# Kernel tuning notes

Hardware: AMD Instinct MI355X
Metric: run time of the kernel (lower is better)

## Reference

```python
import jax, jax.numpy as jnp
import numpy as np

N = 50000          # nodes
E = 1600000        # edges (avg degree 32)
G = 16             # graphs in batch
H = 128            # hidden_dim
HOP = 3
IN_DIM = 1


def setup_inputs() -> dict:
    key = jax.random.key(0)
    ks = jax.random.split(key, 12)
    s = 1.0 / np.sqrt(H)
    return {
        "x": jax.random.normal(ks[0], (N, IN_DIM), jnp.float32),
        "edge_index": jax.random.randint(ks[1], (2, E), 0, N, jnp.int64),
        "edge_attr": jax.random.uniform(ks[2], (E, 1), jnp.float32),
        "batch": jnp.sort(jax.random.randint(ks[3], (N,), 0, G, jnp.int64)),
        "W1": jax.random.normal(ks[4], (HOP, H, IN_DIM), jnp.float32) * s,
        "W2": jax.random.normal(ks[5], (HOP, H, H), jnp.float32) * s,
        "W3": jax.random.normal(ks[6], (HOP, H, H), jnp.float32) * s,
        "W4": jax.random.normal(ks[7], (HOP, H, 1), jnp.float32) * s,
        "W5": jax.random.normal(ks[8], (1, 2 * H), jnp.float32) * s,
        "b5": jnp.zeros((1,), jnp.float32),
        "W6": jax.random.normal(ks[9], (H, H), jnp.float32) * s,
        "W7": jax.random.normal(ks[10], (H, H), jnp.float32) * s,
    }


def reference(x, edge_index, edge_attr, batch, W1, W2, W3, W4, W5, b5, W6, W7):
    row, col = edge_index[0], edge_index[1]
    node_emb = jnp.zeros((N, H), x.dtype)
    for l in range(HOP):
        nfe = x @ W1[l].T                                        # [N,H]
        # gather neighbor embeddings along col, scatter-add to row
        ne_aggr = jax.ops.segment_sum(node_emb[col], row, num_segments=N)
        efe = jax.nn.relu(edge_attr @ W4[l].T)                   # [E,H]
        ee_aggr = jax.ops.segment_sum(efe, row, num_segments=N)  # [N,H]
        node_emb = jax.nn.relu(nfe + ne_aggr @ W2[l].T + ee_aggr @ W3[l].T)
    pooled = jax.ops.segment_sum(node_emb, batch, num_segments=G)  # [G,H]
    sum_emb = pooled @ W6.T                                        # [G,H]
    cat = jax.nn.relu(jnp.concatenate([sum_emb[batch], node_emb @ W7.T], axis=-1))
    return cat @ W5.T + b5                                         # [N,1]
```

## Files before the change

### kernel.cpp

```cpp
#include <hip/hip_runtime.h>
#include <hip/hip_bf16.h>

#define N_NODES 50000
#define N_EDGES 1600000
#define NGRAPH  16
#define HID     128

#define RPB   128
#define NB    ((N_NODES + RPB - 1) / RPB)
#define NBLK  256
#define EPB   ((N_EDGES + NBLK - 1) / NBLK)
#define P4CAP 6144

typedef unsigned int uint32;
typedef unsigned short ushort;
typedef unsigned char uchar;
typedef __attribute__((ext_vector_type(8))) short bf16x8;
typedef __attribute__((ext_vector_type(4))) float f32x4;
typedef __attribute__((ext_vector_type(2))) float f32x2;

__device__ __forceinline__ uint32 bf16r(float f) {
    uint32 b = __float_as_uint(f);
    return (b + 0x7fffu + ((b >> 16) & 1u)) >> 16;
}
__device__ __forceinline__ uint32 pack_bf16(float lo, float hi) {
    return bf16r(lo) | (bf16r(hi) << 16);
}

__global__ __launch_bounds__(1024) void k_p1i(const int* __restrict__ row,
                                              int* __restrict__ blkhist,
                                              float* __restrict__ zp, int nz,
                                              const float* __restrict__ W2,
                                              const float* __restrict__ W7,
                                              const float* __restrict__ W3,
                                              const float* __restrict__ W4,
                                              ushort* __restrict__ wpack,
                                              float* __restrict__ v3) {
    __shared__ int hist[NB];
    int tid = threadIdx.x, blk = blockIdx.x;
    int gid = blk * 1024 + tid;
    if (gid < nz) zp[gid] = 0.f;
    if (gid < 4 * 16384) {
        int m = gid >> 14, f = gid & 16383;
        int j = f & 7, lane = (f >> 3) & 63, kk = (f >> 9) & 3, t = (f >> 11) & 7;
        int hp = t * 16 + (lane & 15);
        int k  = kk * 32 + ((lane >> 4) & 3) * 8 + j;
        const float* src = (m < 3) ? (W2 + m * HID * HID) : W7;
        wpack[gid] = (ushort)bf16r(src[hp * HID + k]);
    }
    if (gid < 3 * HID) {
        int l = gid / HID, hp = gid % HID;
        float acc = 0.f;
        for (int h = 0; h < HID; h++)
            acc += W3[l * HID * HID + hp * HID + h] * fmaxf(W4[l * HID + h], 0.f);
        v3[gid] = acc;
    }
    for (int i = tid; i < NB; i += 1024) hist[i] = 0;
    __syncthreads();
    int s = blk * EPB, e = s + EPB; if (e > N_EDGES) e = N_EDGES;
    for (int i = s + tid; i < e; i += 1024)
        atomicAdd(&hist[row[i] >> 7], 1);
    __syncthreads();
    for (int i = tid; i < NB; i += 1024)
        blkhist[i * NBLK + blk] = hist[i];
}

__global__ __launch_bounds__(NBLK) void k_p2a(int* __restrict__ blkhist,
                                              int* __restrict__ btot) {
    __shared__ int sums[NBLK];
    int t = threadIdx.x, b = blockIdx.x;
    int v = blkhist[b * NBLK + t];
    sums[t] = v;
    __syncthreads();
    for (int d = 1; d < NBLK; d <<= 1) {
        int u = (t >= d) ? sums[t - d] : 0;
        __syncthreads();
        sums[t] += u;
        __syncthreads();
    }
    blkhist[b * NBLK + t] = sums[t] - v;
    if (t == NBLK - 1) btot[b] = sums[t];
}

__global__ __launch_bounds__(1024) void k_p3_part(const int* __restrict__ row,
                                                  const int* __restrict__ col,
                                                  const float* __restrict__ ea,
                                                  const int* __restrict__ blkhist,
                                                  const int* __restrict__ btot,
                                                  int2* __restrict__ pea) {
    __shared__ int sc[512];
    __shared__ int cur[NB];
    int tid = threadIdx.x, blk = blockIdx.x;
    if (tid < 512) sc[tid] = (tid < NB) ? btot[tid] : 0;
    __syncthreads();
    for (int d = 1; d < 512; d <<= 1) {
        int v = 0;
        if (tid < 512 && tid >= d) v = sc[tid - d];
        __syncthreads();
        if (tid < 512) sc[tid] += v;
        __syncthreads();
    }
    for (int i = tid; i < NB; i += 1024)
        cur[i] = (sc[i] - btot[i]) + blkhist[i * NBLK + blk];
    __syncthreads();
    int s = blk * EPB, e = s + EPB; if (e > N_EDGES) e = N_EDGES;
    for (int i = s + tid; i < e; i += 1024) {
        int r = row[i], c = col[i];
        float a = ea[i];
        int slot = atomicAdd(&cur[r >> 7], 1);
        pea[slot] = make_int2(((r & (RPB - 1)) << 16) | c, __float_as_int(a));
    }
}

__global__ __launch_bounds__(512) void k_p4(const int2* __restrict__ pea,
                                            const int* __restrict__ btot,
                                            const float* __restrict__ x,
                                            int* __restrict__ offs,
                                            float* __restrict__ ea_sum,
                                            int* __restrict__ csr,
                                            uchar* __restrict__ emb0,
                                            const float* __restrict__ w1l0,
                                            const float* __restrict__ v3l0) {
    __shared__ int2  cache[P4CAP];
    __shared__ int   red[512];
    __shared__ int   cnt[RPB];
    __shared__ float eas[RPB];
    __shared__ int   scan_s[RPB];
    __shared__ int   curp[RPB];
    int t = threadIdx.x, b = blockIdx.x;
    red[t] = (t < b) ? btot[t] : 0;
    __syncthreads();
    for (int d = 256; d > 0; d >>= 1) {
        if (t < d) red[t] += red[t + d];
        __syncthreads();
    }
    int s = red[0];
    int e = s + btot[b];
    int len = e - s;
    int clen = len < P4CAP ? len : P4CAP;
    for (int i = t; i < clen; i += 512) cache[i] = pea[s + i];
    if (t < RPB) { cnt[t] = 0; eas[t] = 0.f; }
    __syncthreads();
    for (int i = t; i < len; i += 512) {
        int2 p = (i < P4CAP) ? cache[i] : pea[s + i];
        int lr = ((uint32)p.x) >> 16;
        atomicAdd(&cnt[lr], 1);
        atomicAdd(&eas[lr], __int_as_float(p.y));
    }
    __syncthreads();
    if (t < RPB) scan_s[t] = cnt[t];
    __syncthreads();
    for (int d = 1; d < RPB; d <<= 1) {
        int v = 0;
        if (t < RPB && t >= d) v = scan_s[t - d];
        __syncthreads();
        if (t < RPB) scan_s[t] += v;
        __syncthreads();
    }
    int nbase = b * RPB;
    if (t < RPB) {
        int excl = scan_s[t] - cnt[t];
        int n = nbase + t;
        if (n < N_NODES) {
            offs[n] = s + excl;
            ea_sum[n] = eas[t];
        }
        curp[t] = s + excl;
    }
    if (b == NB - 1 && t == 0) offs[N_NODES] = e;
    __syncthreads();
    for (int i = t; i < len; i += 512) {
        int2 p = (i < P4CAP) ? cache[i] : pea[s + i];
        int slot = atomicAdd(&curp[((uint32)p.x) >> 16], 1);
        csr[slot] = p.x & 0xFFFF;
    }
    for (int i = t; i < RPB * 32; i += 512) {
        int lr = i >> 5, c4 = (i & 31) * 4;
        int n = nbase + lr;
        if (n < N_NODES) {
            float xv = x[n];
            float ev = eas[lr];
            float v0 = fmaxf(xv * w1l0[c4 + 0] + ev * v3l0[c4 + 0], 0.f) * 0.015625f;
            float v1 = fmaxf(xv * w1l0[c4 + 1] + ev * v3l0[c4 + 1], 0.f) * 0.015625f;
            float v2 = fmaxf(xv * w1l0[c4 + 2] + ev * v3l0[c4 + 2], 0.f) * 0.015625f;
            float v3v = fmaxf(xv * w1l0[c4 + 3] + ev * v3l0[c4 + 3], 0.f) * 0.015625f;
            int u = __builtin_amdgcn_cvt_pk_fp8_f32(v0, v1, 0, false);
            u = __builtin_amdgcn_cvt_pk_fp8_f32(v2, v3v, u, true);
            *(uint32*)(emb0 + (size_t)n * 128 + c4) = (uint32)u;
        }
    }
}

__global__ __launch_bounds__(256) void k_gather(const uchar* __restrict__ emb,
                                                const int* __restrict__ offs,
                                                const int* __restrict__ csr,
                                                uint32* __restrict__ agg) {
    int node = (blockIdx.x * 256 + threadIdx.x) >> 6;
    int lane = threadIdx.x & 63;
    if (node >= N_NODES) return;
    int hl = lane & 31;
    int half = lane >> 5;
    int boff = hl << 2;
    int s = offs[node], e = offs[node + 1];
    f32x2 a0 = {0.f, 0.f}, a1 = a0, a2 = a0, a3 = a0;
#pragma unroll 1
    for (int base = s; base < e; base += 64) {
        int idx = base + lane;
        int cv = (idx < e) ? csr[idx] : 0;
        int cnt = e - base; if (cnt > 64) cnt = 64;
        int j = 0;
#pragma unroll 1
        for (; j + 16 <= cnt; j += 16) {
            uint32 w[8];
#pragma unroll
            for (int q = 0; q < 8; q++) {
                int c0 = __builtin_amdgcn_readlane(cv, j + 2 * q);
                int c1 = __builtin_amdgcn_readlane(cv, j + 2 * q + 1);
                int c  = half ? c1 : c0;
                w[q] = *(const uint32*)(emb + (((uint32)c) << 7) + boff);
            }
#pragma unroll
            for (int q = 0; q < 8; q++) {
                f32x2 lo = __builtin_amdgcn_cvt_pk_f32_fp8((int)w[q], false);
                f32x2 hi = __builtin_amdgcn_cvt_pk_f32_fp8((int)w[q], true);
                if (q & 1) { a2 += lo; a3 += hi; } else { a0 += lo; a1 += hi; }
            }
        }
#pragma unroll 1
        for (; j + 2 <= cnt; j += 2) {
            int c0 = __builtin_amdgcn_readlane(cv, j);
            int c1 = __builtin_amdgcn_readlane(cv, j + 1);
            int c  = half ? c1 : c0;
            uint32 w = *(const uint32*)(emb + (((uint32)c) << 7) + boff);
            a0 += __builtin_amdgcn_cvt_pk_f32_fp8((int)w, false);
            a1 += __builtin_amdgcn_cvt_pk_f32_fp8((int)w, true);
        }
        if (j < cnt) {
            int c0 = __builtin_amdgcn_readlane(cv, j);
            uint32 w = half ? 0u : *(const uint32*)(emb + (((uint32)c0) << 7) + boff);
            a0 += __builtin_amdgcn_cvt_pk_f32_fp8((int)w, false);
            a1 += __builtin_amdgcn_cvt_pk_f32_fp8((int)w, true);
        }
    }
    a0 += a2; a1 += a3;
    a0.x += __shfl_xor(a0.x, 32); a0.y += __shfl_xor(a0.y, 32);
    a1.x += __shfl_xor(a1.x, 32); a1.y += __shfl_xor(a1.y, 32);
    if (half == 0) {
        uint2 wv2;
        wv2.x = pack_bf16(a0.x * 64.f, a0.y * 64.f);
        wv2.y = pack_bf16(a1.x * 64.f, a1.y * 64.f);
        *(uint2*)(agg + (size_t)node * 64 + hl * 2) = wv2;
    }
}

#define LROW 136

template <bool LAST>
__global__ __launch_bounds__(256) void k_gemm(const uint32* __restrict__ agg,
                                              const ushort* __restrict__ w2p,
                                              const float* __restrict__ w1l,
                                              const float* __restrict__ v3l,
                                              const float* __restrict__ x,
                                              const float* __restrict__ ea_sum,
                                              uchar* __restrict__ emb8Out,
                                              const ushort* __restrict__ w7p,
                                              const float* __restrict__ W5,
                                              float* __restrict__ outp,
                                              const int* __restrict__ batch,
                                              float* __restrict__ pooled) {
    __shared__ ushort tile[64 * LROW];
    __shared__ float redp[4][128];
    int tid = threadIdx.x;
    int tbase = blockIdx.x * 64;
    int wv = tid >> 6, lane = tid & 63;
    int n0 = lane & 15, quad = lane >> 4;
    int arow = wv * 16 + n0;
    bf16x8 a0 = {0,0,0,0,0,0,0,0}, a1 = a0, a2 = a0, a3 = a0;
    if (tbase + arow < N_NODES) {
        const bf16x8* ap = (const bf16x8*)(agg + (size_t)(tbase + arow) * 64);
        a0 = ap[0 + quad]; a1 = ap[4 + quad]; a2 = ap[8 + quad]; a3 = ap[12 + quad];
    }
    const bf16x8* wb = (const bf16x8*)w2p;
    f32x4 acc[8];
#pragma unroll
    for (int t = 0; t < 8; t++) {
        f32x4 c = {0.f, 0.f, 0.f, 0.f};
        c = __builtin_amdgcn_mfma_f32_16x16x32_bf16(a0, wb[(t * 4 + 0) * 64 + lane], c, 0, 0, 0);
        c = __builtin_amdgcn_mfma_f32_16x16x32_bf16(a1, wb[(t * 4 + 1) * 64 + lane], c, 0, 0, 0);
        c = __builtin_amdgcn_mfma_f32_16x16x32_bf16(a2, wb[(t * 4 + 2) * 64 + lane], c, 0, 0, 0);
        c = __builtin_amdgcn_mfma_f32_16x16x32_bf16(a3, wb[(t * 4 + 3) * 64 + lane], c, 0, 0, 0);
        acc[t] = c;
    }
    float xs[4], es[4];
#pragma unroll
    for (int r = 0; r < 4; r++) {
        int n = tbase + wv * 16 + quad * 4 + r;
        xs[r] = (n < N_NODES) ? x[n] : 0.f;
        es[r] = (n < N_NODES) ? ea_sum[n] : 0.f;
    }
    if (!LAST) {
        uchar* stile = (uchar*)tile;
#pragma unroll
        for (int t = 0; t < 8; t++) {
            int hp = t * 16 + n0;
            float w1v = w1l[hp], v3v = v3l[hp];
#pragma unroll
            for (int r = 0; r < 4; r++) {
                float v = fmaxf(acc[t][r] + xs[r] * w1v + es[r] * v3v, 0.f) * 0.015625f;
                int enc = __builtin_amdgcn_cvt_pk_fp8_f32(v, v, 0, false);
                stile[(wv * 16 + quad * 4 + r) * 136 + hp] = (uchar)(enc & 0xff);
            }
        }
        __syncthreads();
        int vn = N_NODES - tbase; if (vn > 64) vn = 64;
        for (int i = tid; i < 64 * 32; i += 256) {
            int r = i >> 5, c4 = (i & 31) * 4;
            if (r < vn) {
                uint32 u = *(const uint32*)&stile[r * 136 + c4];
                *(uint32*)(emb8Out + (size_t)(tbase + r) * 128 + c4) = u;
            }
        }
    } else {
        int nlast = tbase + 63; if (nlast > N_NODES - 1) nlast = N_NODES - 1;
        int g0 = batch[tbase];
        bool uni = (batch[nlast] == g0);
        int gr[4];
        if (!uni) {
#pragma unroll
            for (int r = 0; r < 4; r++) {
                int n = tbase + wv * 16 + quad * 4 + r;
                gr[r] = (n < N_NODES) ? batch[n] : 0;
            }
        }
        float st[8];
#pragma unroll
        for (int t = 0; t < 8; t++) {
            int hp = t * 16 + n0;
            float w1v = w1l[hp], v3v = v3l[hp];
            float stt = 0.f;
#pragma unroll
            for (int r = 0; r < 4; r++) {
                float v = fmaxf(acc[t][r] + xs[r] * w1v + es[r] * v3v, 0.f);
                tile[(wv * 16 + quad * 4 + r) * LROW + hp] = (ushort)bf16r(v);
                if (uni) {
                    stt += v;
                } else {
                    int n = tbase + wv * 16 + quad * 4 + r;
                    if (n < N_NODES) atomicAdd(&pooled[gr[r] * HID + hp], v);
                }
            }
            st[t] = stt;
        }
        if (uni) {
#pragma unroll
            for (int t = 0; t < 8; t++) {
                float v = st[t];
                v += __shfl_xor(v, 16);
                v += __shfl_xor(v, 32);
                if (lane < 16) redp[wv][t * 16 + lane] = v;
            }
        }
        __syncthreads();
        if (uni && tid < 128) {
            float sp = (redp[0][tid] + redp[1][tid]) + (redp[2][tid] + redp[3][tid]);
            atomicAdd(&pooled[g0 * HID + tid], sp);
        }
        bf16x8 b0 = *(const bf16x8*)&tile[arow * LROW + 0 * 32 + quad * 8];
        bf16x8 b1 = *(const bf16x8*)&tile[arow * LROW + 1 * 32 + quad * 8];
        bf16x8 b2 = *(const bf16x8*)&tile[arow * LROW + 2 * 32 + quad * 8];
        bf16x8 b3 = *(const bf16x8*)&tile[arow * LROW + 3 * 32 + quad * 8];
        const bf16x8* w7 = (const bf16x8*)w7p;
        float p[4] = {0.f, 0.f, 0.f, 0.f};
#pragma unroll
        for (int t = 0; t < 8; t++) {
            f32x4 c = {0.f, 0.f, 0.f, 0.f};
            c = __builtin_amdgcn_mfma_f32_16x16x32_bf16(b0, w7[(t * 4 + 0) * 64 + lane], c, 0, 0, 0);
            c = __builtin_amdgcn_mfma_f32_16x16x32_bf16(b1, w7[(t * 4 + 1) * 64 + lane], c, 0, 0, 0);
            c = __builtin_amdgcn_mfma_f32_16x16x32_bf16(b2, w7[(t * 4 + 2) * 64 + lane], c, 0, 0, 0);
            c = __builtin_amdgcn_mfma_f32_16x16x32_bf16(b3, w7[(t * 4 + 3) * 64 + lane], c, 0, 0, 0);
            float w5v = W5[128 + t * 16 + n0];
#pragma unroll
            for (int r = 0; r < 4; r++) p[r] += fmaxf(c[r], 0.f) * w5v;
        }
#pragma unroll
        for (int r = 0; r < 4; r++) {
            float v = p[r];
            v += __shfl_xor(v, 1);
            v += __shfl_xor(v, 2);
            v += __shfl_xor(v, 4);
            v += __shfl_xor(v, 8);
            int n = tbase + wv * 16 + quad * 4 + r;
            if (n0 == 0 && n < N_NODES) outp[n] = v;
        }
    }
}

__global__ __launch_bounds__(256) void k_tail(float* __restrict__ out,
                                              const int* __restrict__ batch,
                                              const float* __restrict__ pooled,
                                              const float* __restrict__ W6,
                                              const float* __restrict__ W5,
                                              const float* __restrict__ b5) {
    __shared__ float red[256];
    __shared__ int gsh[2];
    int t = threadIdx.x;
    int nbase = blockIdx.x * 256;
    int n = nbase + t;
    if (t == 0) gsh[0] = batch[nbase < N_NODES ? nbase : N_NODES - 1];
    if (t == 1) gsh[1] = batch[(nbase + 255) < N_NODES ? (nbase + 255) : N_NODES - 1];
    __syncthreads();
    int g_lo = gsh[0], g_hi = gsh[1];
    int hp = t & 127;
    int g = (t >> 7) ? g_hi : g_lo;
    const float* pg = pooled + g * HID;
    const float* wr = W6 + hp * HID;
    float acc = 0.f;
    for (int h = 0; h < HID; h++) acc += pg[h] * wr[h];
    red[t] = fmaxf(acc, 0.f) * W5[hp];
    __syncthreads();
    for (int d = 64; d > 0; d >>= 1) {
        if (hp < d) red[t] += red[t + d];
        __syncthreads();
    }
    float s_lo = red[0], s_hi = red[128];
    if (n < N_NODES) {
        int gn = batch[n];
        float s;
        if (gn == g_lo) s = s_lo;
        else if (gn == g_hi) s = s_hi;
        else {
            s = 0.f;
            const float* pg2 = pooled + gn * HID;
            for (int hp2 = 0; hp2 < HID; hp2++) {
                float a2 = 0.f;
                for (int h = 0; h < HID; h++) a2 += pg2[h] * W6[hp2 * HID + h];
                s += fmaxf(a2, 0.f) * W5[hp2];
            }
        }
        out[n] += s + b5[0];
    }
}

extern "C" void kernel_launch(void* const* d_in, const int* in_sizes, int n_in,
                              void* d_out, int out_size, void* d_ws, size_t ws_size,
                              hipStream_t stream) {
    (void)in_sizes; (void)n_in; (void)out_size; (void)ws_size;
    const float* x    = (const float*)d_in[0];
    const int*   ei   = (const int*)d_in[1];
    const float* ea   = (const float*)d_in[2];
    const int*   bat  = (const int*)d_in[3];
    const float* W1   = (const float*)d_in[4];
    const float* W2   = (const float*)d_in[5];
    const float* W3   = (const float*)d_in[6];
    const float* W4   = (const float*)d_in[7];
    const float* W5   = (const float*)d_in[8];
    const float* b5   = (const float*)d_in[9];
    const float* W6   = (const float*)d_in[10];
    const float* W7   = (const float*)d_in[11];
    float* out = (float*)d_out;

    const int* row = ei;
    const int* col = ei + N_EDGES;

    float* wsf = (float*)d_ws;
    int*   wsi = (int*)d_ws;
    size_t o = 0;
    float* pooled = wsf + o; o += NGRAPH * HID;
    size_t ztot = o;
    int*   offs   = wsi + o; o += N_NODES + 1;
    float* ea_sum = wsf + o; o += N_NODES;
    int*   btot   = wsi + o; o += NB;
    float* v3     = wsf + o; o += 3 * HID;
    int*   blkh   = wsi + o; o += NB * NBLK;
    o = (o + 3) & ~(size_t)3;
    ushort* wpack = (ushort*)(wsi + o); o += 4 * 16384 / 2;
    int*    csr   = wsi + o; o += N_EDGES;
    o = (o + 1) & ~(size_t)1;
    int2*   pea   = (int2*)(wsi + o); o += 2 * (size_t)N_EDGES;
    uint32* aggB  = (uint32*)(wsi + o); o += (size_t)N_NODES * 64;
    uchar*  emb8  = (uchar*)(wsi + o);  o += (size_t)N_NODES * 32;
    uchar*  emb0  = (uchar*)(wsi + o);  o += (size_t)N_NODES * 32;

    const ushort* w2p1 = wpack + 1 * 16384;
    const ushort* w2p2 = wpack + 2 * 16384;
    const ushort* w7p  = wpack + 3 * 16384;

    k_p1i<<<NBLK, 1024, 0, stream>>>(row, blkh, (float*)d_ws, (int)ztot,
                                     W2, W7, W3, W4, (ushort*)wpack, v3);
    k_p2a<<<NB, NBLK, 0, stream>>>(blkh, btot);
    k_p3_part<<<NBLK, 1024, 0, stream>>>(row, col, ea, blkh, btot, pea);
    k_p4<<<NB, 512, 0, stream>>>(pea, btot, x, offs, ea_sum, csr, emb0, W1, v3);
    k_gather<<<(N_NODES * 64 + 255) / 256, 256, 0, stream>>>(emb0, offs, csr, aggB);
    k_gemm<false><<<(N_NODES + 63) / 64, 256, 0, stream>>>(
        aggB, w2p1, W1 + 1 * HID, v3 + 1 * HID, x, ea_sum, emb8, nullptr, nullptr, nullptr,
        nullptr, nullptr);
    k_gather<<<(N_NODES * 64 + 255) / 256, 256, 0, stream>>>(emb8, offs, csr, aggB);
    k_gemm<true><<<(N_NODES + 63) / 64, 256, 0, stream>>>(
        aggB, w2p2, W1 + 2 * HID, v3 + 2 * HID, x, ea_sum, nullptr, w7p, W5, out, bat, pooled);
    k_tail<<<(N_NODES + 255) / 256, 256, 0, stream>>>(out, bat, pooled, W6, W5, b5);
}
```

Measured before the change: 266.7 us.

## Split fp8 embeddings into two 64-byte halves and gather each half separately

Node embeddings move from one 128-byte row per node to two separate 3.2 MB arrays holding the low and high 64 features. The gather kernel makes two passes, one per half, with 16 lanes per neighbor, so four neighbors are fetched per wave instruction. Each pass touches a smaller array that fits better in L2/MALL, aiming for a higher cache hit rate on the random neighbor reads. The cost is reading the CSR twice, an extra shuffle-reduction level, and a branchier tail loop.

```diff
diff --git a/kernel.cpp b/kernel.cpp
--- a/kernel.cpp
+++ b/kernel.cpp
@@ -118,7 +118,8 @@
                                             int* __restrict__ offs,
                                             float* __restrict__ ea_sum,
                                             int* __restrict__ csr,
-                                            uchar* __restrict__ emb0,
+                                            uchar* __restrict__ emb0Lo,
+                                            uchar* __restrict__ emb0Hi,
                                             const float* __restrict__ w1l0,
                                             const float* __restrict__ v3l0) {
     __shared__ int2  cache[P4CAP];
@@ -186,70 +187,83 @@
             float v3v = fmaxf(xv * w1l0[c4 + 3] + ev * v3l0[c4 + 3], 0.f) * 0.015625f;
             int u = __builtin_amdgcn_cvt_pk_fp8_f32(v0, v1, 0, false);
             u = __builtin_amdgcn_cvt_pk_fp8_f32(v2, v3v, u, true);
-            *(uint32*)(emb0 + (size_t)n * 128 + c4) = (uint32)u;
-        }
-    }
-}
-
-__global__ __launch_bounds__(256) void k_gather(const uchar* __restrict__ emb,
+            uchar* dst = (c4 < 64) ? emb0Lo : emb0Hi;
+            *(uint32*)(dst + (size_t)n * 64 + (c4 & 63)) = (uint32)u;
+        }
+    }
+}
+
+__global__ __launch_bounds__(256) void k_gather(const uchar* __restrict__ embLo,
+                                                const uchar* __restrict__ embHi,
                                                 const int* __restrict__ offs,
                                                 const int* __restrict__ csr,
                                                 uint32* __restrict__ agg) {
     int node = (blockIdx.x * 256 + threadIdx.x) >> 6;
     int lane = threadIdx.x & 63;
     if (node >= N_NODES) return;
-    int hl = lane & 31;
-    int half = lane >> 5;
-    int boff = hl << 2;
+    int q  = lane >> 4;
+    int ql = lane & 15;
+    int boff = ql << 2;
+    bool q0 = (q & 1) != 0, q1 = (q & 2) != 0;
     int s = offs[node], e = offs[node + 1];
-    f32x2 a0 = {0.f, 0.f}, a1 = a0, a2 = a0, a3 = a0;
 #pragma unroll 1
-    for (int base = s; base < e; base += 64) {
-        int idx = base + lane;
-        int cv = (idx < e) ? csr[idx] : 0;
-        int cnt = e - base; if (cnt > 64) cnt = 64;
-        int j = 0;
+    for (int p = 0; p < 2; p++) {
+        const uchar* emb = p ? embHi : embLo;
+        f32x2 a0 = {0.f, 0.f}, a1 = a0, a2 = a0, a3 = a0;
 #pragma unroll 1
-        for (; j + 16 <= cnt; j += 16) {
-            uint32 w[8];
-#pragma unroll
-            for (int q = 0; q < 8; q++) {
-                int c0 = __builtin_amdgcn_readlane(cv, j + 2 * q);
-                int c1 = __builtin_amdgcn_readlane(cv, j + 2 * q + 1);
-                int c  = half ? c1 : c0;
-                w[q] = *(const uint32*)(emb + (((uint32)c) << 7) + boff);
-            }
-#pragma unroll
-            for (int q = 0; q < 8; q++) {
-                f32x2 lo = __builtin_amdgcn_cvt_pk_f32_fp8((int)w[q], false);
-                f32x2 hi = __builtin_amdgcn_cvt_pk_f32_fp8((int)w[q], true);
-                if (q & 1) { a2 += lo; a3 += hi; } else { a0 += lo; a1 += hi; }
-            }
-        }
+        for (int base = s; base < e; base += 64) {
+            int idx = base + lane;
+            int cv = (idx < e) ? csr[idx] : 0;
+            int cnt = e - base; if (cnt > 64) cnt = 64;
+            int j = 0;
 #pragma unroll 1
-        for (; j + 2 <= cnt; j += 2) {
-            int c0 = __builtin_amdgcn_readlane(cv, j);
-            int c1 = __builtin_amdgcn_readlane(cv, j + 1);
-            int c  = half ? c1 : c0;
-            uint32 w = *(const uint32*)(emb + (((uint32)c) << 7) + boff);
-            a0 += __builtin_amdgcn_cvt_pk_f32_fp8((int)w, false);
-            a1 += __builtin_amdgcn_cvt_pk_f32_fp8((int)w, true);
-        }
-        if (j < cnt) {
-            int c0 = __builtin_amdgcn_readlane(cv, j);
-            uint32 w = half ? 0u : *(const uint32*)(emb + (((uint32)c0) << 7) + boff);
-            a0 += __builtin_amdgcn_cvt_pk_f32_fp8((int)w, false);
-            a1 += __builtin_amdgcn_cvt_pk_f32_fp8((int)w, true);
-        }
-    }
-    a0 += a2; a1 += a3;
-    a0.x += __shfl_xor(a0.x, 32); a0.y += __shfl_xor(a0.y, 32);
-    a1.x += __shfl_xor(a1.x, 32); a1.y += __shfl_xor(a1.y, 32);
-    if (half == 0) {
-        uint2 wv2;
-        wv2.x = pack_bf16(a0.x * 64.f, a0.y * 64.f);
-        wv2.y = pack_bf16(a1.x * 64.f, a1.y * 64.f);
-        *(uint2*)(agg + (size_t)node * 64 + hl * 2) = wv2;
+            for (; j + 16 <= cnt; j += 16) {
+                uint32 w[4];
+#pragma unroll
+                for (int u = 0; u < 4; u++) {
+                    int c0 = __builtin_amdgcn_readlane(cv, j + 4 * u + 0);
+                    int c1 = __builtin_amdgcn_readlane(cv, j + 4 * u + 1);
+                    int c2 = __builtin_amdgcn_readlane(cv, j + 4 * u + 2);
+                    int c3 = __builtin_amdgcn_readlane(cv, j + 4 * u + 3);
+                    int clo = q0 ? c1 : c0;
+                    int chi = q0 ? c3 : c2;
+                    int c   = q1 ? chi : clo;
+                    w[u] = *(const uint32*)(emb + (((uint32)c) << 6) + boff);
+                }
+#pragma unroll
+                for (int u = 0; u < 4; u++) {
+                    f32x2 lo = __builtin_amdgcn_cvt_pk_f32_fp8((int)w[u], false);
+                    f32x2 hi = __builtin_amdgcn_cvt_pk_f32_fp8((int)w[u], true);
+                    if (u & 1) { a2 += lo; a3 += hi; } else { a0 += lo; a1 += hi; }
+                }
+            }
+#pragma unroll 1
+            for (; j < cnt; j += 4) {
+                int jm = cnt - 1;
+                int c0 = __builtin_amdgcn_readlane(cv, j);
+                int c1 = __builtin_amdgcn_readlane(cv, (j + 1 < cnt) ? j + 1 : jm);
+                int c2 = __builtin_amdgcn_readlane(cv, (j + 2 < cnt) ? j + 2 : jm);
+                int c3 = __builtin_amdgcn_readlane(cv, (j + 3 < cnt) ? j + 3 : jm);
+                int clo = q0 ? c1 : c0;
+                int chi = q0 ? c3 : c2;
+                int c   = q1 ? chi : clo;
+                uint32 w = *(const uint32*)(emb + (((uint32)c) << 6) + boff);
+                if (j + q >= cnt) w = 0u;
+                a0 += __builtin_amdgcn_cvt_pk_f32_fp8((int)w, false);
+                a1 += __builtin_amdgcn_cvt_pk_f32_fp8((int)w, true);
+            }
+        }
+        a0 += a2; a1 += a3;
+        a0.x += __shfl_xor(a0.x, 16); a0.y += __shfl_xor(a0.y, 16);
+        a1.x += __shfl_xor(a1.x, 16); a1.y += __shfl_xor(a1.y, 16);
+        a0.x += __shfl_xor(a0.x, 32); a0.y += __shfl_xor(a0.y, 32);
+        a1.x += __shfl_xor(a1.x, 32); a1.y += __shfl_xor(a1.y, 32);
+        if (lane < 16) {
+            uint2 wv2;
+            wv2.x = pack_bf16(a0.x * 64.f, a0.y * 64.f);
+            wv2.y = pack_bf16(a1.x * 64.f, a1.y * 64.f);
+            *(uint2*)(agg + (size_t)node * 64 + p * 32 + ql * 2) = wv2;
+        }
     }
 }
 
@@ -262,7 +276,8 @@
                                               const float* __restrict__ v3l,
                                               const float* __restrict__ x,
                                               const float* __restrict__ ea_sum,
-                                              uchar* __restrict__ emb8Out,
+                                              uchar* __restrict__ emb8Lo,
+                                              uchar* __restrict__ emb8Hi,
                                               const ushort* __restrict__ w7p,
                                               const float* __restrict__ W5,
                                               float* __restrict__ outp,
@@ -317,7 +332,8 @@
             int r = i >> 5, c4 = (i & 31) * 4;
             if (r < vn) {
                 uint32 u = *(const uint32*)&stile[r * 136 + c4];
-                *(uint32*)(emb8Out + (size_t)(tbase + r) * 128 + c4) = u;
+                uchar* dst = (c4 < 64) ? emb8Lo : emb8Hi;
+                *(uint32*)(dst + (size_t)(tbase + r) * 64 + (c4 & 63)) = u;
             }
         }
     } else {
@@ -478,8 +494,10 @@
     o = (o + 1) & ~(size_t)1;
     int2*   pea   = (int2*)(wsi + o); o += 2 * (size_t)N_EDGES;
     uint32* aggB  = (uint32*)(wsi + o); o += (size_t)N_NODES * 64;
-    uchar*  emb8  = (uchar*)(wsi + o);  o += (size_t)N_NODES * 32;
-    uchar*  emb0  = (uchar*)(wsi + o);  o += (size_t)N_NODES * 32;
+    uchar*  emb8Lo = (uchar*)(wsi + o); o += (size_t)N_NODES * 16;
+    uchar*  emb8Hi = (uchar*)(wsi + o); o += (size_t)N_NODES * 16;
+    uchar*  emb0Lo = (uchar*)(wsi + o); o += (size_t)N_NODES * 16;
+    uchar*  emb0Hi = (uchar*)(wsi + o); o += (size_t)N_NODES * 16;
 
     const ushort* w2p1 = wpack + 1 * 16384;
     const ushort* w2p2 = wpack + 2 * 16384;
@@ -489,13 +507,14 @@
                                      W2, W7, W3, W4, (ushort*)wpack, v3);
     k_p2a<<<NB, NBLK, 0, stream>>>(blkh, btot);
     k_p3_part<<<NBLK, 1024, 0, stream>>>(row, col, ea, blkh, btot, pea);
-    k_p4<<<NB, 512, 0, stream>>>(pea, btot, x, offs, ea_sum, csr, emb0, W1, v3);
-    k_gather<<<(N_NODES * 64 + 255) / 256, 256, 0, stream>>>(emb0, offs, csr, aggB);
+    k_p4<<<NB, 512, 0, stream>>>(pea, btot, x, offs, ea_sum, csr, emb0Lo, emb0Hi, W1, v3);
+    k_gather<<<(N_NODES * 64 + 255) / 256, 256, 0, stream>>>(emb0Lo, emb0Hi, offs, csr, aggB);
     k_gemm<false><<<(N_NODES + 63) / 64, 256, 0, stream>>>(
-        aggB, w2p1, W1 + 1 * HID, v3 + 1 * HID, x, ea_sum, emb8, nullptr, nullptr, nullptr,
-        nullptr, nullptr);
-    k_gather<<<(N_NODES * 64 + 255) / 256, 256, 0, stream>>>(emb8, offs, csr, aggB);
+        aggB, w2p1, W1 + 1 * HID, v3 + 1 * HID, x, ea_sum, emb8Lo, emb8Hi,
+        nullptr, nullptr, nullptr, nullptr, nullptr);
+    k_gather<<<(N_NODES * 64 + 255) / 256, 256, 0, stream>>>(emb8Lo, emb8Hi, offs, csr, aggB);
     k_gemm<true><<<(N_NODES + 63) / 64, 256, 0, stream>>>(
-        aggB, w2p2, W1 + 2 * HID, v3 + 2 * HID, x, ea_sum, nullptr, w7p, W5, out, bat, pooled);
+        aggB, w2p2, W1 + 2 * HID, v3 + 2 * HID, x, ea_sum, nullptr, nullptr,
+        w7p, W5, out, bat, pooled);
     k_tail<<<(N_NODES + 255) / 256, 256, 0, stream>>>(out, bat, pooled, W6, W5, b5);
 }
```

Measured after the change: 293.0 us. +9.8%, slower.
